# Performance work log

Measured on AMD Instinct MI355X. Metric: run time of the kernel, lower is better.

The kernel has to match this reference:

```python
import jax, jax.numpy as jnp
import numpy as np
import math

N = 100000      # num_of_nodes
E = 1600000     # edges (~avg degree 16)
F = 128         # node_feature
D = 128         # node_hidden (also topK pool size)
NR = 90000      # remaining nodes
L = 2           # num_conv_layer
LAMDA = 0.5
ALPHA = 0.1


def setup_inputs() -> dict:
    key = jax.random.key(0)
    ks = jax.random.split(key, 12)
    g = lambda k, s: jax.random.normal(k, s, jnp.float32) * 0.05
    perm = np.random.RandomState(0).permutation(N)  # disjoint remain/added split
    return {
        "x": jax.random.normal(ks[0], (N, F), jnp.float32),
        "node_scores": jax.random.normal(ks[1], (N,), jnp.float32),
        "W_hid": g(ks[2], (F, D)), "b_hid": jnp.zeros((D,), jnp.float32),
        "Wl": g(ks[3], (D, D)), "bl": jnp.zeros((D,), jnp.float32),
        "Wr": g(ks[4], (D, D)), "br": jnp.zeros((D,), jnp.float32),
        "a": g(ks[5], (1, D)),
        "h0_w": g(ks[6], (D, D)),              # initial_weight (GRU hidden init / GCN weight)
        "W_ih": g(ks[7], (3 * D, D)), "W_hh": g(ks[8], (3 * D, D)),
        "b_ih": jnp.zeros((3 * D,), jnp.float32), "b_hh": jnp.zeros((3 * D,), jnp.float32),
        "edge_index": jax.random.randint(ks[9], (2, E), 0, N),
        "remain_nodes_index": jnp.asarray(perm[:NR], jnp.int32),
        "added_nodes_index": jnp.asarray(perm[NR:], jnp.int32),
        "node_id": jnp.arange(N, dtype=jnp.int32),
    }


def _gru_step(x_in, h, W_ih, W_hh, b_ih, b_hh):
    # torch nn.GRU single step, gate order (r, z, n)
    gx = x_in @ W_ih.T + b_ih
    gh = h @ W_hh.T + b_hh
    xr, xz, xn = jnp.split(gx, 3, axis=-1)
    hr, hz, hn = jnp.split(gh, 3, axis=-1)
    r = jax.nn.sigmoid(xr + hr)
    z = jax.nn.sigmoid(xz + hz)
    n = jnp.tanh(xn + r * hn)
    return (1.0 - z) * n + z * h


def _edge_softmax_weights(edge_index, a, h_l, h_r):
    # _dynamic_self_attention_v2: per-edge scores normalized over src rows
    src, dst = edge_index[0], edge_index[1]
    al = (jax.nn.leaky_relu(h_l, 0.2) * a).sum(-1)   # [N]
    ar = (jax.nn.leaky_relu(h_r, 0.2) * a).sum(-1)   # [N]
    e = al[src] + ar[dst]                            # [E]
    e = jnp.exp(e - e.max())
    rowsum = jax.ops.segment_sum(e, src, num_segments=h_l.shape[0])
    return e / (rowsum[src] + 1e-16)


def _spmm_adj_t(edge_index, w, feats):
    # (A_trans @ feats)[i] = sum over edges with dst==i of w_e * feats[src]
    src, dst = edge_index[0], edge_index[1]
    return jax.ops.segment_sum(w[:, None] * feats[src], dst, num_segments=feats.shape[0])


def reference(x, node_scores, W_hid, b_hid, Wl, bl, Wr, br, a, h0_w, W_ih, W_hh, b_ih, b_hh, edge_index, remain_nodes_index, added_nodes_index, node_id):
    h = jax.nn.relu(x @ W_hid + b_hid)                 # [N, D]
    remain_nodes = node_id[remain_nodes_index]
    remain_x = h[remain_nodes_index]
    added_nodes = node_id[added_nodes_index]
    added_x = h[added_nodes_index]
    scores = node_scores[remain_nodes_index]
    X_res = jnp.zeros((N, D), h.dtype)
    X_res = X_res.at[remain_nodes].set(remain_x).at[added_nodes].set(added_x)
    # topK pooling branch (N > D and NR > D statically)
    _, topk = jax.lax.top_k(scores, D)
    X_pool = remain_x[topk]                            # [D, D]: GRU batch=D, feat=D
    pooling_node = remain_nodes[topk]
    h_new = _gru_step(X_pool, h0_w, W_ih, W_hh, b_ih, b_hh)  # [D, D]
    # torch: X_GCN = X_residual (alias) then in-place scatter -> both updated
    X_res = X_res.at[pooling_node].set(h_new)
    X_gcn = X_res
    Wl_X = jax.nn.relu(X_gcn @ Wl + bl)
    Wr_X = jax.nn.relu(X_gcn @ Wr + br)
    w_edge = _edge_softmax_weights(edge_index, a, Wl_X, Wr_X)
    out = X_gcn
    for l in range(1, L + 1):
        theta = math.log(LAMDA / l + 1.0)
        hi = _spmm_adj_t(edge_index, w_edge, out)
        support = (1.0 - ALPHA) * hi + ALPHA * X_res
        out = jax.nn.relu(theta * (support @ h_new) + (1.0 - theta) * support)
    return out
```

## Files before the change

### kernel.cpp

```cpp
#include <hip/hip_runtime.h>

typedef unsigned int u32;
typedef unsigned short u16;
typedef unsigned long long u64;

#define DD 128
#define ELLW 64
#define NB 196
#define BSH 9
#define BCAP 12288

typedef __attribute__((ext_vector_type(8))) short short8;
typedef __attribute__((ext_vector_type(4))) float f32x4;
union fragu { uint4 q; short8 s; };

__device__ __forceinline__ u32 mono32(float f) {
    u32 u = __float_as_uint(f);
    return (u & 0x80000000u) ? ~u : (u | 0x80000000u);
}
__device__ __forceinline__ u16 f2bf(float f) {
    u32 u = __float_as_uint(f);
    u32 r = (u + 0x7FFFu + ((u >> 16) & 1u)) >> 16;
    return (u16)r;
}
__device__ __forceinline__ float bflo(u32 p) { return __uint_as_float(p << 16); }
__device__ __forceinline__ float bfhi(u32 p) { return __uint_as_float(p & 0xFFFF0000u); }
__device__ __forceinline__ u32 packbf(float a, float b) {
    return (u32)f2bf(a) | ((u32)f2bf(b) << 16);
}

__device__ u32 block_incl_scan(u32 v, u32* wsum ) {
    int t = threadIdx.x, lane = t & 63, wid = t >> 6;
    u32 sc = v;
#pragma unroll
    for (int off = 1; off < 64; off <<= 1) {
        u32 n1 = __shfl_up(sc, off);
        if (lane >= off) sc += n1;
    }
    if (lane == 63) wsum[wid] = sc;
    __syncthreads();
    if (t < 16) {
        u32 wv = wsum[t];
#pragma unroll
        for (int off = 1; off < 16; off <<= 1) {
            u32 n1 = __shfl_up(wv, off, 16);
            if ((t & 15) >= off) wv += n1;
        }
        wsum[t] = wv;
    }
    __syncthreads();
    u32 r = sc + (wid ? wsum[wid - 1] : 0u);
    __syncthreads();
    return r;
}

template <int MODE, int ABF>
__global__ __launch_bounds__(256) void k_mfma(
    const void* __restrict__ Ain, const u32* __restrict__ resid,
    const float* __restrict__ B, const float* __restrict__ bias,
    const float* __restrict__ av, const float* __restrict__ scaleS,
    u16* __restrict__ outBF, float* __restrict__ outF, float* __restrict__ outS,
    float theta, int N) {
    __shared__ alignas(16) unsigned char As[64 * 256];
    __shared__ float spart[64];
    int t = threadIdx.x, lane = t & 63, wave = t >> 6;
    int R0 = blockIdx.x * 64;
    int brow = (lane >> 4) * 8;
    int bcol0 = wave * 32 + (lane & 15);
    fragu bfr[2][4];
#pragma unroll
    for (int ntl = 0; ntl < 2; ++ntl)
#pragma unroll
        for (int ks = 0; ks < 4; ++ks) {
            u16 h[8];
#pragma unroll
            for (int i = 0; i < 8; ++i)
                h[i] = f2bf(B[(size_t)(ks * 32 + brow + i) * 128 + bcol0 + ntl * 16]);
            bfr[ntl][ks].q = make_uint4((u32)h[0] | ((u32)h[1] << 16), (u32)h[2] | ((u32)h[3] << 16),
                                        (u32)h[4] | ((u32)h[5] << 16), (u32)h[6] | ((u32)h[7] << 16));
        }
    float bc[2] = {0.f, 0.f}, ac[2] = {0.f, 0.f};
    if (MODE == 0 || MODE == 1) {
#pragma unroll
        for (int ntl = 0; ntl < 2; ++ntl) {
            bc[ntl] = bias[bcol0 + ntl * 16];
            if (MODE == 1) ac[ntl] = av[bcol0 + ntl * 16];
        }
    }
    if (MODE == 1 && t < 64) spart[t] = 0.f;
#pragma unroll
    for (int q2 = 0; q2 < 4; ++q2) {
        int c = t + q2 * 256;
        int row = c >> 4, c16 = c & 15;
        uint4 v = make_uint4(0u, 0u, 0u, 0u);
        if (R0 + row < N) {
            if (ABF == 1) {
                v = ((const uint4*)Ain)[(size_t)(R0 + row) * 16 + c16];
            } else if (ABF == 2) {
                uint4 pv = ((const uint4*)Ain)[(size_t)(R0 + row) * 16 + c16];
                uint4 xv = ((const uint4*)resid)[(size_t)(R0 + row) * 16 + c16];
                v.x = packbf(bflo(pv.x) + 0.1f * bflo(xv.x), bfhi(pv.x) + 0.1f * bfhi(xv.x));
                v.y = packbf(bflo(pv.y) + 0.1f * bflo(xv.y), bfhi(pv.y) + 0.1f * bfhi(xv.y));
                v.z = packbf(bflo(pv.z) + 0.1f * bflo(xv.z), bfhi(pv.z) + 0.1f * bfhi(xv.z));
                v.w = packbf(bflo(pv.w) + 0.1f * bflo(xv.w), bfhi(pv.w) + 0.1f * bfhi(xv.w));
            } else {
                float4 f0 = ((const float4*)Ain)[(size_t)(R0 + row) * 32 + c16 * 2];
                float4 f1 = ((const float4*)Ain)[(size_t)(R0 + row) * 32 + c16 * 2 + 1];
                v.x = packbf(f0.x, f0.y);
                v.y = packbf(f0.z, f0.w);
                v.z = packbf(f1.x, f1.y);
                v.w = packbf(f1.z, f1.w);
            }
        }
        *(uint4*)(As + row * 256 + ((c16 * 16) ^ ((row & 7) << 4))) = v;
    }
    __syncthreads();
    int arow = lane & 15, agrp = lane >> 4;
    float om = 1.f - theta;
#pragma unroll
    for (int rs = 0; rs < 4; ++rs) {
        int rl = rs * 16 + arow;
        fragu afr[4];
#pragma unroll
        for (int ks = 0; ks < 4; ++ks)
            afr[ks].q = *(const uint4*)(As + rl * 256 + ((ks * 64 + agrp * 16) ^ ((rl & 7) << 4)));
        float part[4] = {0.f, 0.f, 0.f, 0.f};
#pragma unroll
        for (int ntl = 0; ntl < 2; ++ntl) {
            f32x4 acc = {0.f, 0.f, 0.f, 0.f};
#pragma unroll
            for (int ks = 0; ks < 4; ++ks)
                acc = __builtin_amdgcn_mfma_f32_16x16x32_bf16(afr[ks].s, bfr[ntl][ks].s, acc, 0, 0, 0);
            int colg = wave * 32 + ntl * 16 + (lane & 15);
#pragma unroll
            for (int r = 0; r < 4; ++r) {
                int rowg = R0 + rs * 16 + agrp * 4 + r;
                if (MODE == 0) {
                    float v = fmaxf(acc[r] + bc[ntl], 0.f);
                    if (rowg < N) outBF[(size_t)rowg * 128 + colg] = f2bf(v);
                } else if (MODE == 1) {
                    part[r] += fmaxf(acc[r] + bc[ntl], 0.f) * ac[ntl];
                } else {
                    int rl2 = rs * 16 + agrp * 4 + r;
                    u16 rh = *(const u16*)(As + rl2 * 256 + ((colg * 2) ^ ((rl2 & 7) << 4)));
                    float resv = __uint_as_float((u32)rh << 16);
                    float v = fmaxf(theta * acc[r] + om * resv, 0.f);
                    if (rowg < N) {
                        if (MODE == 2) {
                            float rsc = 1.f / (scaleS[rowg] + 1e-30f);
                            outBF[(size_t)rowg * 128 + colg] = f2bf(v * rsc);
                        } else {
                            outF[(size_t)rowg * 128 + colg] = v;
                        }
                    }
                }
            }
        }
        if (MODE == 1) {
#pragma unroll
            for (int r = 0; r < 4; ++r) {
                float s = part[r];
                s += __shfl_xor(s, 1); s += __shfl_xor(s, 2);
                s += __shfl_xor(s, 4); s += __shfl_xor(s, 8);
                if ((lane & 15) == 0) atomicAdd(&spart[rs * 16 + agrp * 4 + r], s);
            }
        }
    }
    if (MODE == 1) {
        __syncthreads();
        if (t < 64 && R0 + t < N) outS[R0 + t] = expf(spart[t]);
    }
}

__global__ __launch_bounds__(256) void k_spmm(
    const u32* __restrict__ feat, const float* __restrict__ ear,
    const u32* __restrict__ cnt, const int* __restrict__ ell,
    u32* __restrict__ P, int N) {
    int w = (int)((blockIdx.x * (u32)blockDim.x + threadIdx.x) >> 6);
    int lane = threadIdx.x & 63;
    if (w >= N) return;
    int m = (int)min(cnt[w], (u32)ELLW);
    int sv = (lane < m) ? ell[((size_t)w << 6) + lane] : 0;
    float a0 = 0.f, a1 = 0.f;
    int j = 0;
    for (; j + 8 <= m; j += 8) {
        int s0 = __shfl(sv, j + 0), s1 = __shfl(sv, j + 1);
        int s2 = __shfl(sv, j + 2), s3 = __shfl(sv, j + 3);
        int s4 = __shfl(sv, j + 4), s5 = __shfl(sv, j + 5);
        int s6 = __shfl(sv, j + 6), s7 = __shfl(sv, j + 7);
        u32 p0 = feat[(size_t)s0 * 64 + lane];
        u32 p1 = feat[(size_t)s1 * 64 + lane];
        u32 p2 = feat[(size_t)s2 * 64 + lane];
        u32 p3 = feat[(size_t)s3 * 64 + lane];
        u32 p4 = feat[(size_t)s4 * 64 + lane];
        u32 p5 = feat[(size_t)s5 * 64 + lane];
        u32 p6 = feat[(size_t)s6 * 64 + lane];
        u32 p7 = feat[(size_t)s7 * 64 + lane];
        a0 += bflo(p0) + bflo(p1) + bflo(p2) + bflo(p3) + bflo(p4) + bflo(p5) + bflo(p6) + bflo(p7);
        a1 += bfhi(p0) + bfhi(p1) + bfhi(p2) + bfhi(p3) + bfhi(p4) + bfhi(p5) + bfhi(p6) + bfhi(p7);
    }
    for (; j + 2 <= m; j += 2) {
        int s0 = __shfl(sv, j + 0), s1 = __shfl(sv, j + 1);
        u32 p0 = feat[(size_t)s0 * 64 + lane];
        u32 p1 = feat[(size_t)s1 * 64 + lane];
        a0 += bflo(p0) + bflo(p1);
        a1 += bfhi(p0) + bfhi(p1);
    }
    if (j < m) {
        int s0 = __shfl(sv, j);
        u32 p0 = feat[(size_t)s0 * 64 + lane];
        a0 += bflo(p0);
        a1 += bfhi(p0);
    }
    float sc = 0.9f * ear[w];
    P[(size_t)w * 64 + lane] = packbf(sc * a0, sc * a1);
}

__global__ void k_init(u32* __restrict__ curD, u32* __restrict__ curS) {
    int t = blockIdx.x * blockDim.x + threadIdx.x;
    if (t < NB) { curD[t] = (u32)t * BCAP; curS[t] = (u32)t * BCAP; }
}

__global__ __launch_bounds__(256) void k_bucket(
    const int* __restrict__ ei, u32* __restrict__ bD, u32* __restrict__ bS,
    u32* __restrict__ curD, u32* __restrict__ curS, int E, int nblocks) {
    __shared__ u32 cnt0[NB], cnt1[NB], pos0[NB], pos1[NB], base0[NB], base1[NB];
    int t = threadIdx.x;
    int chunk = (E + nblocks - 1) / nblocks;
    int e0 = blockIdx.x * chunk, e1 = min(E, e0 + chunk);
    for (int i = t; i < NB; i += 256) { cnt0[i] = 0; cnt1[i] = 0; pos0[i] = 0; pos1[i] = 0; }
    __syncthreads();
    for (int e = e0 + t; e < e1; e += 256) {
        int s = ei[e], d = ei[E + e];
        atomicAdd(&cnt0[d >> BSH], 1u);
        atomicAdd(&cnt1[s >> BSH], 1u);
    }
    __syncthreads();
    for (int i = t; i < NB; i += 256) {
        base0[i] = atomicAdd(&curD[i], cnt0[i]);
        base1[i] = atomicAdd(&curS[i], cnt1[i]);
    }
    __syncthreads();
    for (int e = e0 + t; e < e1; e += 256) {
        int s = ei[e], d = ei[E + e];
        int bd = d >> BSH, bs = s >> BSH;
        u32 pD = base0[bd] + atomicAdd(&pos0[bd], 1u);
        u32 pS = base1[bs] + atomicAdd(&pos1[bs], 1u);
        if (pD < (u32)(bd + 1) * BCAP) bD[pD] = ((u32)(d & 511) << 17) | (u32)s;
        if (pS < (u32)(bs + 1) * BCAP) bS[pS] = ((u32)(s & 511) << 17) | (u32)d;
    }
}

__global__ __launch_bounds__(256) void k_ellSsc(
    const u32* __restrict__ bD, const u32* __restrict__ bS,
    const u32* __restrict__ curD, const u32* __restrict__ curS,
    const float* __restrict__ ear, const u32* __restrict__ Xrbf,
    int* __restrict__ ell, u32* __restrict__ cnt,
    float* __restrict__ S, u32* __restrict__ Xsc, int N) {
    __shared__ u32 lcnt[512];
    __shared__ float ls[512];
    int t = threadIdx.x;
    if (blockIdx.x < NB) {
        int b = blockIdx.x;
        for (int i = t; i < 512; i += 256) lcnt[i] = 0;
        __syncthreads();
        u32 beg = (u32)b * BCAP, end = curD[b];
        for (u32 e = beg + t; e < end; e += 256) {
            u32 p = bD[e];
            int dloc = (int)(p >> 17), s = (int)(p & 0x1FFFFu);
            u32 q = atomicAdd(&lcnt[dloc], 1u);
            if (q < (u32)ELLW) ell[(((size_t)(b << BSH) + dloc) << 6) + q] = s;
        }
        __syncthreads();
        int r0 = b << BSH;
        for (int i = t; i < 512; i += 256) {
            int row = r0 + i;
            if (row < N) cnt[row] = min(lcnt[i], (u32)ELLW);
        }
    } else {
        int b = blockIdx.x - NB;
        for (int i = t; i < 512; i += 256) ls[i] = 0.f;
        __syncthreads();
        u32 beg = (u32)b * BCAP, end = curS[b];
        for (u32 e = beg + t; e < end; e += 256) {
            u32 p = bS[e];
            int sloc = (int)(p >> 17), d = (int)(p & 0x1FFFFu);
            atomicAdd(&ls[sloc], ear[d]);
        }
        __syncthreads();
        int r0 = b << BSH;
        for (int i = t; i < 512; i += 256) {
            int row = r0 + i;
            if (row < N) S[row] = ls[i];
        }
        int rows = min(512, N - r0);
        if (rows <= 0) return;
        for (int idx = t; idx < rows * 64; idx += 256) {
            int rl = idx >> 6, c = idx & 63;
            int row = r0 + rl;
            float rs = 1.f / (ls[rl] + 1e-30f);
            u32 p = Xrbf[(size_t)row * 64 + c];
            Xsc[(size_t)row * 64 + c] = packbf(bflo(p) * rs, bfhi(p) * rs);
        }
    }
}

__global__ void k_hist(const float* __restrict__ scores, const int* __restrict__ remain,
                       u32* __restrict__ hist, int NR) {
    int i = blockIdx.x * blockDim.x + threadIdx.x;
    if (i < NR) atomicAdd(&hist[mono32(scores[remain[i]]) >> 16], 1u);
}

__global__ void k_cutoff(const u32* __restrict__ hist, u32* __restrict__ misc, int K) {
    __shared__ u32 wsum[16];
    __shared__ u32 carry_s, found_s;
    int t = threadIdx.x;
    if (t == 0) { carry_s = 0; found_s = 0; }
    __syncthreads();
    for (int c = 0; c < 64; ++c) {
        int key = 65535 - ((c << 10) + t);
        u32 v = hist[key];
        u32 carry = carry_s;
        __syncthreads();
        u32 incl = block_incl_scan(v, wsum);
        u32 mycum = carry + incl;
        u32 myprev = mycum - v;
        if (mycum >= (u32)K && myprev < (u32)K) {
            misc[2] = (u32)key;
            misc[3] = myprev;
            found_s = 1;
        }
        if (t == 1023) carry_s = mycum;
        __syncthreads();
        if (found_s) return;
    }
}

__global__ void k_collect(const float* __restrict__ scores, const int* __restrict__ remain,
                          const u32* __restrict__ misc, int* __restrict__ cand,
                          u32* __restrict__ cand_cnt, int NR, int CMAX) {
    u32 B = misc[2];
    int i = blockIdx.x * blockDim.x + threadIdx.x;
    if (i < NR) {
        u32 b = mono32(scores[remain[i]]) >> 16;
        if (b >= B) {
            u32 p = atomicAdd(cand_cnt, 1u);
            if (p < (u32)CMAX) cand[p] = i;
        }
    }
}

__global__ void k_select(const float* __restrict__ scores, const int* __restrict__ remain,
                         const u32* __restrict__ misc, const int* __restrict__ cand,
                         int* __restrict__ pooling, int K, int CMAX) {
    __shared__ u64 keys[4096];
    int n = (int)min(misc[0], (u32)CMAX);
    int t = threadIdx.x;
    for (int c = t; c < n; c += 1024) {
        int i = cand[c];
        u32 m = mono32(scores[remain[i]]);
        keys[c] = ((u64)m << 32) | (u64)(0xFFFFFFFFu - (u32)i);
    }
    __syncthreads();
    for (int c = t; c < n; c += 1024) {
        u64 myk = keys[c];
        int rank = 0;
        for (int j = 0; j < n; ++j) rank += (keys[j] > myk) ? 1 : 0;
        if (rank < K) pooling[rank] = remain[cand[c]];
    }
}

__global__ void k_gru(const u16* __restrict__ Xh, const int* __restrict__ pooling,
                      const float* __restrict__ h0w, const float* __restrict__ Wih,
                      const float* __restrict__ Whh, const float* __restrict__ bih,
                      const float* __restrict__ bhh, float* __restrict__ hnew) {
    __shared__ float xrow[DD], hrow[DD];
    int j = blockIdx.x, t = threadIdx.x;
    int node = pooling[j];
    xrow[t] = __uint_as_float((u32)Xh[(size_t)node * DD + t] << 16);
    hrow[t] = h0w[j * DD + t];
    __syncthreads();
    float gx[3], gh[3];
#pragma unroll
    for (int g = 0; g < 3; ++g) {
        const float* wi = Wih + (g * DD + t) * DD;
        const float* wh = Whh + (g * DD + t) * DD;
        float ax = bih[g * DD + t];
        float ah = bhh[g * DD + t];
        for (int d = 0; d < DD; ++d) {
            ax += xrow[d] * wi[d];
            ah += hrow[d] * wh[d];
        }
        gx[g] = ax; gh[g] = ah;
    }
    float r = 1.f / (1.f + expf(-(gx[0] + gh[0])));
    float z = 1.f / (1.f + expf(-(gx[1] + gh[1])));
    float nn = tanhf(gx[2] + r * gh[2]);
    hnew[j * DD + t] = (1.f - z) * nn + z * hrow[t];
}

__global__ void k_scatter(u32* __restrict__ Xr_bf, const int* __restrict__ pooling,
                          const float* __restrict__ hnew) {
    int j = blockIdx.x, t = threadIdx.x;
    int row = pooling[j];
    float2 f = ((const float2*)hnew)[j * 64 + t];
    Xr_bf[(size_t)row * 64 + t] = packbf(f.x, f.y);
}

extern "C" void kernel_launch(void* const* d_in, const int* in_sizes, int n_in,
                              void* d_out, int out_size, void* d_ws, size_t ws_size,
                              hipStream_t stream) {
    const float* x    = (const float*)d_in[0];
    const float* nsc  = (const float*)d_in[1];
    const float* Wh   = (const float*)d_in[2];
    const float* bh   = (const float*)d_in[3];
    const float* Wr   = (const float*)d_in[6];
    const float* br   = (const float*)d_in[7];
    const float* av   = (const float*)d_in[8];
    const float* h0w  = (const float*)d_in[9];
    const float* Wih  = (const float*)d_in[10];
    const float* Whh  = (const float*)d_in[11];
    const float* bih  = (const float*)d_in[12];
    const float* bhh  = (const float*)d_in[13];
    const int* ei     = (const int*)d_in[14];
    const int* remain = (const int*)d_in[15];

    int N = in_sizes[1];
    int E = in_sizes[14] / 2;
    int NR = in_sizes[15];
    const int K = DD;
    const int CMAX = 4096;
    int mblocks = (N + 63) / 64;
    const int NBLK = 512;

    char* ws = (char*)d_ws;
    size_t off = 0;
    auto alloc = [&](size_t bytes) -> size_t {
        off = (off + 255) & ~(size_t)255;
        size_t o = off;
        off += bytes;
        return o;
    };
    size_t bucket_bytes = (size_t)2 * NB * BCAP * 4;
    size_t sup_bytes = (size_t)N * 64 * 4;
    size_t o_Xrbf = alloc((size_t)N * 64 * 4);
    size_t o_Xsc  = alloc((size_t)N * 64 * 4);
    size_t o_Abf  = alloc((size_t)N * 64 * 4);
    size_t o_sup  = alloc(bucket_bytes > sup_bytes ? bucket_bytes : sup_bytes);
    size_t o_ear  = alloc((size_t)N * 4);
    size_t o_ell  = alloc((size_t)N * ELLW * 4);
    size_t o_cand = alloc((size_t)CMAX * 4);
    size_t o_pool = alloc((size_t)K * 4);
    size_t o_hnew = alloc((size_t)DD * DD * 4);
    size_t o_S    = alloc((size_t)N * 4);
    size_t o_cnt  = alloc((size_t)N * 4);
    size_t o_cur  = alloc((size_t)2 * 256 * 4);
    size_t o_hist = alloc((size_t)65536 * 4);
    size_t o_misc = alloc((size_t)64 * 4);
    size_t zero_len = (o_misc + 64 * 4) - o_hist;
    (void)ws_size; (void)n_in; (void)out_size;

    u32*   Xrbf = (u32*)(ws + o_Xrbf);
    u32*   Xsc  = (u32*)(ws + o_Xsc);
    u32*   Abf  = (u32*)(ws + o_Abf);
    u32*   P    = (u32*)(ws + o_sup);
    u32*   bD   = (u32*)(ws + o_sup);
    u32*   bS   = (u32*)(ws + o_sup + (size_t)NB * BCAP * 4);
    float* ear  = (float*)(ws + o_ear);
    int*   ell  = (int*)(ws + o_ell);
    int*   cand = (int*)(ws + o_cand);
    int*   pool = (int*)(ws + o_pool);
    float* hnew = (float*)(ws + o_hnew);
    float* S    = (float*)(ws + o_S);
    u32*   cnt  = (u32*)(ws + o_cnt);
    u32*   curD = (u32*)(ws + o_cur);
    u32*   curS = (u32*)(ws + o_cur + 256 * 4);
    u32*   hist = (u32*)(ws + o_hist);
    u32*   misc = (u32*)(ws + o_misc);

    const float theta1 = 0.40546510810816438f;
    const float theta2 = 0.22314355131420976f;

    hipMemsetAsync(ws + o_hist, 0, zero_len, stream);

    k_mfma<0, 0><<<mblocks, 256, 0, stream>>>(x, nullptr, Wh, bh, nullptr, nullptr,
                                              (u16*)Xrbf, nullptr, nullptr, 0.f, N);
    k_hist<<<(NR + 255) / 256, 256, 0, stream>>>(nsc, remain, hist, NR);
    k_cutoff<<<1, 1024, 0, stream>>>(hist, misc, K);
    k_collect<<<(NR + 255) / 256, 256, 0, stream>>>(nsc, remain, misc, cand, misc, NR, CMAX);
    k_select<<<1, 1024, 0, stream>>>(nsc, remain, misc, cand, pool, K, CMAX);
    k_gru<<<K, DD, 0, stream>>>((const u16*)Xrbf, pool, h0w, Wih, Whh, bih, bhh, hnew);
    k_scatter<<<K, 64, 0, stream>>>(Xrbf, pool, hnew);
    k_mfma<1, 1><<<mblocks, 256, 0, stream>>>(Xrbf, nullptr, Wr, br, av, nullptr,
                                              nullptr, nullptr, ear, 0.f, N);
    k_init<<<1, 256, 0, stream>>>(curD, curS);
    k_bucket<<<NBLK, 256, 0, stream>>>(ei, bD, bS, curD, curS, E, NBLK);
    k_ellSsc<<<2 * NB, 256, 0, stream>>>(bD, bS, curD, curS, ear, Xrbf, ell, cnt, S, Xsc, N);
    k_spmm<<<(N + 3) / 4, 256, 0, stream>>>(Xsc, ear, cnt, ell, P, N);
    k_mfma<2, 2><<<mblocks, 256, 0, stream>>>(P, Xrbf, hnew, nullptr, nullptr, S,
                                              (u16*)Abf, nullptr, nullptr, theta1, N);
    k_spmm<<<(N + 3) / 4, 256, 0, stream>>>(Abf, ear, cnt, ell, P, N);
    k_mfma<3, 2><<<mblocks, 256, 0, stream>>>(P, Xrbf, hnew, nullptr, nullptr, nullptr,
                                              nullptr, (float*)d_out, nullptr, theta2, N);
}
```

Before: 380.1 us.

## Fuse pooled-row scatter and ear fixup into GRU, drop init kernel, unroll SpMM

```diff
diff --git a/kernel.cpp b/kernel.cpp
--- a/kernel.cpp
+++ b/kernel.cpp
@@ -54,7 +54,7 @@
     return r;
 }
 
-template <int MODE, int ABF>
+template <int MODE, int ABF, int EAR>
 __global__ __launch_bounds__(256) void k_mfma(
     const void* __restrict__ Ain, const u32* __restrict__ resid,
     const float* __restrict__ B, const float* __restrict__ bias,
@@ -80,14 +80,14 @@
                                         (u32)h[4] | ((u32)h[5] << 16), (u32)h[6] | ((u32)h[7] << 16));
         }
     float bc[2] = {0.f, 0.f}, ac[2] = {0.f, 0.f};
-    if (MODE == 0 || MODE == 1) {
+    if (MODE == 0) {
 #pragma unroll
         for (int ntl = 0; ntl < 2; ++ntl) {
             bc[ntl] = bias[bcol0 + ntl * 16];
-            if (MODE == 1) ac[ntl] = av[bcol0 + ntl * 16];
-        }
-    }
-    if (MODE == 1 && t < 64) spart[t] = 0.f;
+            if (EAR) ac[ntl] = av[bcol0 + ntl * 16];
+        }
+    }
+    if (EAR && t < 64) spart[t] = 0.f;
 #pragma unroll
     for (int q2 = 0; q2 < 4; ++q2) {
         int c = t + q2 * 256;
@@ -138,8 +138,7 @@
                 if (MODE == 0) {
                     float v = fmaxf(acc[r] + bc[ntl], 0.f);
                     if (rowg < N) outBF[(size_t)rowg * 128 + colg] = f2bf(v);
-                } else if (MODE == 1) {
-                    part[r] += fmaxf(acc[r] + bc[ntl], 0.f) * ac[ntl];
+                    if (EAR) part[r] += v * ac[ntl];
                 } else {
                     int rl2 = rs * 16 + agrp * 4 + r;
                     u16 rh = *(const u16*)(As + rl2 * 256 + ((colg * 2) ^ ((rl2 & 7) << 4)));
@@ -156,7 +155,7 @@
                 }
             }
         }
-        if (MODE == 1) {
+        if (EAR) {
 #pragma unroll
             for (int r = 0; r < 4; ++r) {
                 float s = part[r];
@@ -166,7 +165,7 @@
             }
         }
     }
-    if (MODE == 1) {
+    if (EAR) {
         __syncthreads();
         if (t < 64 && R0 + t < N) outS[R0 + t] = expf(spart[t]);
     }
@@ -183,21 +182,25 @@
     int sv = (lane < m) ? ell[((size_t)w << 6) + lane] : 0;
     float a0 = 0.f, a1 = 0.f;
     int j = 0;
+    for (; j + 16 <= m; j += 16) {
+        u32 pv[16];
+#pragma unroll
+        for (int q = 0; q < 16; ++q) {
+            int s = __shfl(sv, j + q);
+            pv[q] = feat[(size_t)s * 64 + lane];
+        }
+#pragma unroll
+        for (int q = 0; q < 16; ++q) { a0 += bflo(pv[q]); a1 += bfhi(pv[q]); }
+    }
     for (; j + 8 <= m; j += 8) {
-        int s0 = __shfl(sv, j + 0), s1 = __shfl(sv, j + 1);
-        int s2 = __shfl(sv, j + 2), s3 = __shfl(sv, j + 3);
-        int s4 = __shfl(sv, j + 4), s5 = __shfl(sv, j + 5);
-        int s6 = __shfl(sv, j + 6), s7 = __shfl(sv, j + 7);
-        u32 p0 = feat[(size_t)s0 * 64 + lane];
-        u32 p1 = feat[(size_t)s1 * 64 + lane];
-        u32 p2 = feat[(size_t)s2 * 64 + lane];
-        u32 p3 = feat[(size_t)s3 * 64 + lane];
-        u32 p4 = feat[(size_t)s4 * 64 + lane];
-        u32 p5 = feat[(size_t)s5 * 64 + lane];
-        u32 p6 = feat[(size_t)s6 * 64 + lane];
-        u32 p7 = feat[(size_t)s7 * 64 + lane];
-        a0 += bflo(p0) + bflo(p1) + bflo(p2) + bflo(p3) + bflo(p4) + bflo(p5) + bflo(p6) + bflo(p7);
-        a1 += bfhi(p0) + bfhi(p1) + bfhi(p2) + bfhi(p3) + bfhi(p4) + bfhi(p5) + bfhi(p6) + bfhi(p7);
+        u32 pv[8];
+#pragma unroll
+        for (int q = 0; q < 8; ++q) {
+            int s = __shfl(sv, j + q);
+            pv[q] = feat[(size_t)s * 64 + lane];
+        }
+#pragma unroll
+        for (int q = 0; q < 8; ++q) { a0 += bflo(pv[q]); a1 += bfhi(pv[q]); }
     }
     for (; j + 2 <= m; j += 2) {
         int s0 = __shfl(sv, j + 0), s1 = __shfl(sv, j + 1);
@@ -214,11 +217,6 @@
     }
     float sc = 0.9f * ear[w];
     P[(size_t)w * 64 + lane] = packbf(sc * a0, sc * a1);
-}
-
-__global__ void k_init(u32* __restrict__ curD, u32* __restrict__ curS) {
-    int t = blockIdx.x * blockDim.x + threadIdx.x;
-    if (t < NB) { curD[t] = (u32)t * BCAP; curS[t] = (u32)t * BCAP; }
 }
 
 __global__ __launch_bounds__(256) void k_bucket(
@@ -246,8 +244,8 @@
         int bd = d >> BSH, bs = s >> BSH;
         u32 pD = base0[bd] + atomicAdd(&pos0[bd], 1u);
         u32 pS = base1[bs] + atomicAdd(&pos1[bs], 1u);
-        if (pD < (u32)(bd + 1) * BCAP) bD[pD] = ((u32)(d & 511) << 17) | (u32)s;
-        if (pS < (u32)(bs + 1) * BCAP) bS[pS] = ((u32)(s & 511) << 17) | (u32)d;
+        if (pD < (u32)BCAP) bD[(size_t)bd * BCAP + pD] = ((u32)(d & 511) << 17) | (u32)s;
+        if (pS < (u32)BCAP) bS[(size_t)bs * BCAP + pS] = ((u32)(s & 511) << 17) | (u32)d;
     }
 }
 
@@ -264,7 +262,7 @@
         int b = blockIdx.x;
         for (int i = t; i < 512; i += 256) lcnt[i] = 0;
         __syncthreads();
-        u32 beg = (u32)b * BCAP, end = curD[b];
+        u32 beg = (u32)b * BCAP, end = beg + min(curD[b], (u32)BCAP);
         for (u32 e = beg + t; e < end; e += 256) {
             u32 p = bD[e];
             int dloc = (int)(p >> 17), s = (int)(p & 0x1FFFFu);
@@ -281,7 +279,7 @@
         int b = blockIdx.x - NB;
         for (int i = t; i < 512; i += 256) ls[i] = 0.f;
         __syncthreads();
-        u32 beg = (u32)b * BCAP, end = curS[b];
+        u32 beg = (u32)b * BCAP, end = beg + min(curS[b], (u32)BCAP);
         for (u32 e = beg + t; e < end; e += 256) {
             u32 p = bS[e];
             int sloc = (int)(p >> 17), d = (int)(p & 0x1FFFFu);
@@ -370,14 +368,17 @@
     }
 }
 
-__global__ void k_gru(const u16* __restrict__ Xh, const int* __restrict__ pooling,
+__global__ void k_gru(u32* __restrict__ Xr_bf, const int* __restrict__ pooling,
                       const float* __restrict__ h0w, const float* __restrict__ Wih,
                       const float* __restrict__ Whh, const float* __restrict__ bih,
-                      const float* __restrict__ bhh, float* __restrict__ hnew) {
-    __shared__ float xrow[DD], hrow[DD];
+                      const float* __restrict__ bhh, const float* __restrict__ Wr,
+                      const float* __restrict__ br, const float* __restrict__ av,
+                      float* __restrict__ hnew, float* __restrict__ ear) {
+    __shared__ float xrow[DD], hrow[DD], hn[DD];
+    __shared__ float red[2];
     int j = blockIdx.x, t = threadIdx.x;
     int node = pooling[j];
-    xrow[t] = __uint_as_float((u32)Xh[(size_t)node * DD + t] << 16);
+    xrow[t] = __uint_as_float((u32)((const u16*)Xr_bf)[(size_t)node * DD + t] << 16);
     hrow[t] = h0w[j * DD + t];
     __syncthreads();
     float gx[3], gh[3];
@@ -396,15 +397,19 @@
     float r = 1.f / (1.f + expf(-(gx[0] + gh[0])));
     float z = 1.f / (1.f + expf(-(gx[1] + gh[1])));
     float nn = tanhf(gx[2] + r * gh[2]);
-    hnew[j * DD + t] = (1.f - z) * nn + z * hrow[t];
-}
-
-__global__ void k_scatter(u32* __restrict__ Xr_bf, const int* __restrict__ pooling,
-                          const float* __restrict__ hnew) {
-    int j = blockIdx.x, t = threadIdx.x;
-    int row = pooling[j];
-    float2 f = ((const float2*)hnew)[j * 64 + t];
-    Xr_bf[(size_t)row * 64 + t] = packbf(f.x, f.y);
+    float hv = (1.f - z) * nn + z * hrow[t];
+    hnew[j * DD + t] = hv;
+    hn[t] = hv;
+    __syncthreads();
+    if (t < 64) Xr_bf[(size_t)node * 64 + t] = packbf(hn[2 * t], hn[2 * t + 1]);
+    float acc = br[t];
+    for (int k = 0; k < DD; ++k) acc += hn[k] * Wr[k * DD + t];
+    float val = fmaxf(acc, 0.f) * av[t];
+#pragma unroll
+    for (int off = 32; off > 0; off >>= 1) val += __shfl_xor(val, off);
+    if ((t & 63) == 0) red[t >> 6] = val;
+    __syncthreads();
+    if (t == 0) ear[node] = expf(red[0] + red[1]);
 }
 
 extern "C" void kernel_launch(void* const* d_in, const int* in_sizes, int n_in,
@@ -457,7 +462,7 @@
     size_t o_cur  = alloc((size_t)2 * 256 * 4);
     size_t o_hist = alloc((size_t)65536 * 4);
     size_t o_misc = alloc((size_t)64 * 4);
-    size_t zero_len = (o_misc + 64 * 4) - o_hist;
+    size_t zero_len = (o_misc + 64 * 4) - o_cur;
     (void)ws_size; (void)n_in; (void)out_size;
 
     u32*   Xrbf = (u32*)(ws + o_Xrbf);
@@ -481,25 +486,24 @@
     const float theta1 = 0.40546510810816438f;
     const float theta2 = 0.22314355131420976f;
 
-    hipMemsetAsync(ws + o_hist, 0, zero_len, stream);
-
-    k_mfma<0, 0><<<mblocks, 256, 0, stream>>>(x, nullptr, Wh, bh, nullptr, nullptr,
-                                              (u16*)Xrbf, nullptr, nullptr, 0.f, N);
+    hipMemsetAsync(ws + o_cur, 0, zero_len, stream);
+
+    k_mfma<0, 0, 1><<<mblocks, 256, 0, stream>>>(x, nullptr, Wh, bh, av, nullptr,
+                                                 (u16*)Xrbf, nullptr, ear, 0.f, N);
     k_hist<<<(NR + 255) / 256, 256, 0, stream>>>(nsc, remain, hist, NR);
     k_cutoff<<<1, 1024, 0, stream>>>(hist, misc, K);
     k_collect<<<(NR + 255) / 256, 256, 0, stream>>>(nsc, remain, misc, cand, misc, NR, CMAX);
     k_select<<<1, 1024, 0, stream>>>(nsc, remain, misc, cand, pool, K, CMAX);
-    k_gru<<<K, DD, 0, stream>>>((const u16*)Xrbf, pool, h0w, Wih, Whh, bih, bhh, hnew);
-    k_scatter<<<K, 64, 0, stream>>>(Xrbf, pool, hnew);
-    k_mfma<1, 1><<<mblocks, 256, 0, stream>>>(Xrbf, nullptr, Wr, br, av, nullptr,
-                                              nullptr, nullptr, ear, 0.f, N);
-    k_init<<<1, 256, 0, stream>>>(curD, curS);
+    k_mfma<0, 1, 1><<<mblocks, 256, 0, stream>>>(Xrbf, nullptr, Wr, br, av, nullptr,
+                                                 (u16*)Xsc ,
+                                                 nullptr, ear, 0.f, N);
+    k_gru<<<K, DD, 0, stream>>>(Xrbf, pool, h0w, Wih, Whh, bih, bhh, Wr, br, av, hnew, ear);
     k_bucket<<<NBLK, 256, 0, stream>>>(ei, bD, bS, curD, curS, E, NBLK);
     k_ellSsc<<<2 * NB, 256, 0, stream>>>(bD, bS, curD, curS, ear, Xrbf, ell, cnt, S, Xsc, N);
     k_spmm<<<(N + 3) / 4, 256, 0, stream>>>(Xsc, ear, cnt, ell, P, N);
-    k_mfma<2, 2><<<mblocks, 256, 0, stream>>>(P, Xrbf, hnew, nullptr, nullptr, S,
-                                              (u16*)Abf, nullptr, nullptr, theta1, N);
+    k_mfma<2, 2, 0><<<mblocks, 256, 0, stream>>>(P, Xrbf, hnew, nullptr, nullptr, S,
+                                                 (u16*)Abf, nullptr, nullptr, theta1, N);
     k_spmm<<<(N + 3) / 4, 256, 0, stream>>>(Abf, ear, cnt, ell, P, N);
-    k_mfma<3, 2><<<mblocks, 256, 0, stream>>>(P, Xrbf, hnew, nullptr, nullptr, nullptr,
-                                              nullptr, (float*)d_out, nullptr, theta2, N);
-}
+    k_mfma<3, 2, 0><<<mblocks, 256, 0, stream>>>(P, Xrbf, hnew, nullptr, nullptr, nullptr,
+                                                 nullptr, (float*)d_out, nullptr, theta2, N);
+}
```

After: 384.2 us. About the same (+1.1%).
